# Kernel tuning notes

Measured on AMD Instinct MI355X. Metric: run time of the kernel, lower is better.

The kernel has to match this reference:

```python
import jax, jax.numpy as jnp
import numpy as np

B, T, C = 1, 4096, 2048
NH, HS, NQG = 16, 128, 4          # n_head, head_size, n_query_groups (GQA)
Q_PER_KV = NH // NQG              # 4
QKV_DIM = (NH + 2 * NQG) * HS     # 3072
ROT = HS // 2                     # rotary half-dim = 64


def setup_inputs() -> dict:
    key = jax.random.key(0)
    k0, k1, k2 = jax.random.split(key, 3)
    x = jax.random.normal(k0, (B, T, C), dtype=jnp.float32)
    W_attn = jax.random.normal(k1, (QKV_DIM, C), dtype=jnp.float32) * 0.02
    W_proj = jax.random.normal(k2, (C, C), dtype=jnp.float32) * 0.02
    # RoPE cache: cos/sin of shape (T, head_size/2), flash-attn convention
    inv_freq = 1.0 / (10000.0 ** (jnp.arange(0, HS, 2, dtype=jnp.float32) / HS))
    freqs = jnp.arange(T, dtype=jnp.float32)[:, None] * inv_freq[None, :]
    return {"x": x, "cos": jnp.cos(freqs), "sin": jnp.sin(freqs),
            "W_attn": W_attn, "W_proj": W_proj}


def _apply_rope(t, cos, sin):
    # t: (B, T, H, HS); cos/sin: (T, ROT). Non-interleaved (rotate-half) form.
    x1, x2 = t[..., :ROT], t[..., ROT:]
    c = cos[None, :, None, :]
    s = sin[None, :, None, :]
    return jnp.concatenate([x1 * c - x2 * s, x2 * c + x1 * s], axis=-1)


def reference(x, cos, sin, W_attn, W_proj):
    Bx, Tx, Cx = x.shape
    qkv = jnp.einsum('btc,fc->btf', x, W_attn)                 # (B,T,3072)
    qkv = qkv.reshape(Bx, Tx, NQG, Q_PER_KV + 2, HS)
    q = qkv[:, :, :, :Q_PER_KV, :].reshape(Bx, Tx, NH, HS)     # (B,T,16,128)
    k = qkv[:, :, :, Q_PER_KV, :]                              # (B,T,4,128)
    v = qkv[:, :, :, Q_PER_KV + 1, :]                          # (B,T,4,128)
    q = _apply_rope(q, cos, sin)
    k = _apply_rope(k, cos, sin)
    # GQA: expand kv groups to match query heads (repeat_interleave on head dim)
    k = jnp.repeat(k, Q_PER_KV, axis=2)                        # (B,T,16,128)
    v = jnp.repeat(v, Q_PER_KV, axis=2)
    scale = 1.0 / np.sqrt(HS).astype(np.float32)
    scores = jnp.einsum('bthd,bshd->bhts', q, k) * scale       # (B,H,T,T)
    causal = jnp.tril(jnp.ones((Tx, Tx), dtype=bool))
    scores = jnp.where(causal[None, None], scores, jnp.finfo(scores.dtype).min)
    attn = jax.nn.softmax(scores, axis=-1)
    y = jnp.einsum('bhts,bshd->bthd', attn, v).reshape(Bx, Tx, Cx)
    return jnp.einsum('btc,oc->bto', y, W_proj)
```

## Files before the change

kernel.cpp:

```cpp
#include <hip/hip_runtime.h>
#include <hip/hip_bf16.h>

typedef __hip_bfloat16 bf16;
typedef __attribute__((ext_vector_type(8))) short short8;
typedef __attribute__((ext_vector_type(4))) short short4v;
typedef __attribute__((ext_vector_type(4))) float floatx4;

#define T_SEQ 4096
#define C_DIM 2048
#define NHEAD 16
#define HSZ   128
#define NGRP  4

#define MFMA_BF16(A,B,C) __builtin_amdgcn_mfma_f32_16x16x32_bf16((A),(B),(C),0,0,0)

__device__ __forceinline__ void gld_lds16(const bf16* g, bf16* l) {
  __builtin_amdgcn_global_load_lds(
      (__attribute__((address_space(1))) void*)(g),
      (__attribute__((address_space(3))) void*)(l), 16, 0, 0);
}

__global__ void cvt_kernel(const float* __restrict__ src, bf16* __restrict__ dst, long n)
{
  const long i = ((long)blockIdx.x * blockDim.x + threadIdx.x) * 8;
  if (i >= n) return;
  const float4 a = *(const float4*)(src + i);
  const float4 b = *(const float4*)(src + i + 4);
  bf16 tmp[8];
  tmp[0] = __float2bfloat16(a.x); tmp[1] = __float2bfloat16(a.y);
  tmp[2] = __float2bfloat16(a.z); tmp[3] = __float2bfloat16(a.w);
  tmp[4] = __float2bfloat16(b.x); tmp[5] = __float2bfloat16(b.y);
  tmp[6] = __float2bfloat16(b.z); tmp[7] = __float2bfloat16(b.w);
  *(short8*)(dst + i) = *(const short8*)tmp;
}

__global__ __launch_bounds__(256, 3)
void gemm_bt_kernel(const bf16* __restrict__ A, const bf16* __restrict__ B,
                    float* __restrict__ Cf, bf16* __restrict__ Cq,
                    bf16* __restrict__ Ck, bf16* __restrict__ Cvt,
                    int K, int qkv_mode)
{
  __shared__ alignas(16) bf16 As[128 * 64];
  __shared__ alignas(16) bf16 Bs[128 * 64];

  const int t  = threadIdx.x;
  const int w  = t >> 6, l = t & 63;
  const int wr = w >> 1, wc = w & 1;
  const int q4 = l >> 4, ln = l & 15;
  const long bm = (long)blockIdx.y * 128;
  const long bn = (long)blockIdx.x * 128;

  floatx4 acc[4][4] = {};

  const bf16* Ab = A + (bm + t / 8) * (long)K + (t % 8) * 8;
  const bf16* Bb = B + (bn + t / 8) * (long)K + (t % 8) * 8;

  for (int k0 = 0; k0 < K; k0 += 64) {
    __syncthreads();
#pragma unroll
    for (int i = 0; i < 4; ++i) {
      gld_lds16(Ab + (long)i * 32 * K + k0, As + (i * 256 + w * 64) * 8);
      gld_lds16(Bb + (long)i * 32 * K + k0, Bs + (i * 256 + w * 64) * 8);
    }
    __syncthreads();
#pragma unroll
    for (int kk = 0; kk < 64; kk += 32) {
      short8 af[4], bfr[4];
      const int co = kk + q4 * 8;
#pragma unroll
      for (int mi = 0; mi < 4; ++mi)
        af[mi] = *(const short8*)(As + (wr * 64 + mi * 16 + ln) * 64 + co);
#pragma unroll
      for (int ni = 0; ni < 4; ++ni)
        bfr[ni] = *(const short8*)(Bs + (wc * 64 + ni * 16 + ln) * 64 + co);
#pragma unroll
      for (int mi = 0; mi < 4; ++mi)
#pragma unroll
        for (int ni = 0; ni < 4; ++ni)
          acc[mi][ni] = MFMA_BF16(af[mi], bfr[ni], acc[mi][ni]);
    }
  }

  if (!qkv_mode) {
#pragma unroll
    for (int mi = 0; mi < 4; ++mi) {
      const long r0 = bm + wr * 64 + mi * 16 + q4 * 4;
#pragma unroll
      for (int ni = 0; ni < 4; ++ni) {
        const long c = bn + wc * 64 + ni * 16 + ln;
#pragma unroll
        for (int r = 0; r < 4; ++r)
          Cf[(r0 + r) * C_DIM + c] = acc[mi][ni][r];
      }
    }
  } else {
    const int cb = blockIdx.x;
    const int g = cb / 6, slot = cb - g * 6;
    if (slot == 5) {
      bf16* dstv = Cvt + (long)g * HSZ * T_SEQ;
#pragma unroll
      for (int pass = 0; pass < 2; ++pass) {
        __syncthreads();
        if (wc == pass) {
#pragma unroll
          for (int mi = 0; mi < 4; ++mi) {
            const int tc = wr * 64 + mi * 16 + q4 * 4;
#pragma unroll
            for (int ni = 0; ni < 4; ++ni) {
              const int dr = ni * 16 + ln;
              short4v pk;
#pragma unroll
              for (int r = 0; r < 4; ++r) {
                bf16 v = __float2bfloat16(acc[mi][ni][r]);
                pk[r] = *(short*)&v;
              }
              *(short4v*)(As + dr * 128 + tc) = pk;
            }
          }
        }
        __syncthreads();
        const int row = t >> 2, ch = (t & 3) * 32;
        bf16* gp = dstv + (long)(pass * 64 + row) * T_SEQ + bm + ch;
#pragma unroll
        for (int jj = 0; jj < 4; ++jj)
          *(short8*)(gp + jj * 8) = *(const short8*)(As + row * 128 + ch + jj * 8);
      }
    } else {
      bf16* dst = (slot < 4) ? (Cq + (long)(g * 4 + slot) * T_SEQ * HSZ)
                             : (Ck + (long)g * T_SEQ * HSZ);
#pragma unroll
      for (int mi = 0; mi < 4; ++mi) {
        const long r0 = bm + wr * 64 + mi * 16 + q4 * 4;
#pragma unroll
        for (int ni = 0; ni < 4; ++ni) {
          const long c = wc * 64 + ni * 16 + ln;
#pragma unroll
          for (int r = 0; r < 4; ++r)
            dst[(r0 + r) * HSZ + c] = __float2bfloat16(acc[mi][ni][r]);
        }
      }
    }
  }
}

__global__ void rope_kernel(bf16* __restrict__ Q, bf16* __restrict__ Kb,
                            const float* __restrict__ cs, const float* __restrict__ sn)
{
  const long idx = (long)blockIdx.x * blockDim.x + threadIdx.x;
  const long NQ = (long)NHEAD * T_SEQ * 8;
  bf16* buf; long rem; float qs;
  if (idx < NQ) { buf = Q;  rem = idx;      qs = 0.08838834764831845f * 1.4426950408889634f; }
  else          { buf = Kb; rem = idx - NQ; qs = 1.0f; }
  const int d0 = (int)(rem & 7) * 8;
  const int tt = (int)((rem >> 3) & (T_SEQ - 1));
  const int hh = (int)(rem >> 15);
  const float4 c0 = *(const float4*)(cs + tt * 64 + d0);
  const float4 c1 = *(const float4*)(cs + tt * 64 + d0 + 4);
  const float4 s0 = *(const float4*)(sn + tt * 64 + d0);
  const float4 s1 = *(const float4*)(sn + tt * 64 + d0 + 4);
  float cc[8] = {c0.x,c0.y,c0.z,c0.w,c1.x,c1.y,c1.z,c1.w};
  float ss[8] = {s0.x,s0.y,s0.z,s0.w,s1.x,s1.y,s1.z,s1.w};
  bf16* p = buf + ((long)hh * T_SEQ + tt) * HSZ + d0;
  short8 v1 = *(const short8*)(p);
  short8 v2 = *(const short8*)(p + 64);
  short8 o1, o2;
#pragma unroll
  for (int jj = 0; jj < 8; ++jj) {
    short u1 = v1[jj], u2 = v2[jj];
    const float x1 = __bfloat162float(*(bf16*)&u1);
    const float x2 = __bfloat162float(*(bf16*)&u2);
    bf16 y1 = __float2bfloat16((x1 * cc[jj] - x2 * ss[jj]) * qs);
    bf16 y2 = __float2bfloat16((x2 * cc[jj] + x1 * ss[jj]) * qs);
    o1[jj] = *(short*)&y1; o2[jj] = *(short*)&y2;
  }
  *(short8*)(p)      = o1;
  *(short8*)(p + 64) = o2;
}

__global__ __launch_bounds__(256, 2)
void attn_kernel(const bf16* __restrict__ Qg, const bf16* __restrict__ Kg,
                 const bf16* __restrict__ Vtg, bf16* __restrict__ Y)
{
  __shared__ alignas(16) bf16 Ks[64][132];
  __shared__ alignas(16) bf16 Vt[128][68];
  __shared__ alignas(16) bf16 Ps[128][68];

  const int h = blockIdx.y;
  const int p = (blockIdx.y < 8) ? blockIdx.x : (31 - blockIdx.x);
  const int g = h >> 2;
  const int t = threadIdx.x;
  const int w = t >> 6, l = t & 63;
  const int q4 = l >> 4, ln = l & 15;

  const bf16* Qh = Qg + (long)h * T_SEQ * HSZ;
  const bf16* Kh = Kg + (long)g * T_SEQ * HSZ;
  const bf16* Vh = Vtg + (long)g * HSZ * T_SEQ;

  const int qbase = p * 128 + w * 32;

  short8 qf[2][4];
#pragma unroll
  for (int mi = 0; mi < 2; ++mi) {
    const long row = qbase + mi * 16 + ln;
#pragma unroll
    for (int ks = 0; ks < 4; ++ks)
      qf[mi][ks] = *(const short8*)(Qh + row * HSZ + ks * 32 + q4 * 8);
  }

  short8 ones_f;
#pragma unroll
  for (int i = 0; i < 8; ++i) ones_f[i] = (ln == 0) ? (short)0x3F80 : (short)0;

  floatx4 acc[2][8] = {};
  floatx4 acc_l[2] = {};

  const int krow = t >> 4, kc = (t & 15) * 8;
  const int vrow = t >> 3, vc = (t & 7) * 8;

  short8 kpre[4], vpre[4];
#pragma unroll
  for (int i = 0; i < 4; ++i) {
    kpre[i] = *(const short8*)(Kh + (long)(krow + 16 * i) * HSZ + kc);
    vpre[i] = *(const short8*)(Vh + (long)(vrow + 32 * i) * T_SEQ + vc);
  }

  const int jmax = 2 * p + 1;
  for (int j = 0; j <= jmax; ++j) {
    const int s0 = j * 64;
#pragma unroll
    for (int i = 0; i < 4; ++i) {
      *(short8*)(&Ks[krow + 16 * i][kc]) = kpre[i];
      *(short8*)(&Vt[vrow + 32 * i][vc]) = vpre[i];
    }
    __syncthreads();
    if (j < jmax) {
      const int s1 = s0 + 64;
#pragma unroll
      for (int i = 0; i < 4; ++i) {
        kpre[i] = *(const short8*)(Kh + (long)(s1 + krow + 16 * i) * HSZ + kc);
        vpre[i] = *(const short8*)(Vh + (long)(vrow + 32 * i) * T_SEQ + s1 + vc);
      }
    }

    if (s0 <= qbase + 31) {
      floatx4 sacc[2][4] = {};
#pragma unroll
      for (int ks = 0; ks < 4; ++ks) {
        short8 kf[4];
#pragma unroll
        for (int ni = 0; ni < 4; ++ni)
          kf[ni] = *(const short8*)(&Ks[ni * 16 + ln][ks * 32 + q4 * 8]);
#pragma unroll
        for (int mi = 0; mi < 2; ++mi)
#pragma unroll
          for (int ni = 0; ni < 4; ++ni)
            sacc[mi][ni] = MFMA_BF16(qf[mi][ks], kf[ni], sacc[mi][ni]);
      }

#pragma unroll
      for (int mi = 0; mi < 2; ++mi) {
        const int base_m = qbase + mi * 16 + q4 * 4 - s0 - ln;
#pragma unroll
        for (int ni = 0; ni < 4; ++ni)
#pragma unroll
          for (int r = 0; r < 4; ++r) {
            float pv = __builtin_amdgcn_exp2f(sacc[mi][ni][r]);
            if (base_m + r - ni * 16 < 0) pv = 0.f;
            Ps[w * 32 + mi * 16 + q4 * 4 + r][ni * 16 + ln] = __float2bfloat16(pv);
          }
      }

#pragma unroll
      for (int ks = 0; ks < 2; ++ks) {
        short8 pf[2], vf[8];
#pragma unroll
        for (int mi = 0; mi < 2; ++mi)
          pf[mi] = *(const short8*)(&Ps[w * 32 + mi * 16 + ln][ks * 32 + q4 * 8]);
#pragma unroll
        for (int nd = 0; nd < 8; ++nd)
          vf[nd] = *(const short8*)(&Vt[nd * 16 + ln][ks * 32 + q4 * 8]);
#pragma unroll
        for (int mi = 0; mi < 2; ++mi) {
          acc_l[mi] = MFMA_BF16(pf[mi], ones_f, acc_l[mi]);
#pragma unroll
          for (int nd = 0; nd < 8; ++nd)
            acc[mi][nd] = MFMA_BF16(pf[mi], vf[nd], acc[mi][nd]);
        }
      }
    }
    __syncthreads();
  }

#pragma unroll
  for (int mi = 0; mi < 2; ++mi) {
#pragma unroll
    for (int r = 0; r < 4; ++r) {
      const float lv = __shfl(acc_l[mi][r], l & 48, 64);
      const float inv = (lv > 0.f) ? 1.f / lv : 0.f;
      const long tq = qbase + mi * 16 + q4 * 4 + r;
#pragma unroll
      for (int nd = 0; nd < 8; ++nd)
        Y[tq * C_DIM + h * HSZ + nd * 16 + ln] = __float2bfloat16(acc[mi][nd][r] * inv);
    }
  }
}

extern "C" void kernel_launch(void* const* d_in, const int* in_sizes, int n_in,
                              void* d_out, int out_size, void* d_ws, size_t ws_size,
                              hipStream_t stream)
{
  const float* x  = (const float*)d_in[0];
  const float* cs = (const float*)d_in[1];
  const float* sn = (const float*)d_in[2];
  const float* Wa = (const float*)d_in[3];
  const float* Wp = (const float*)d_in[4];
  float* out = (float*)d_out;

  const long nx  = (long)T_SEQ * C_DIM;
  const long nwa = (long)(NHEAD + 2 * NGRP) * HSZ * C_DIM;
  const long nwp = (long)C_DIM * C_DIM;
  const long nqh = (long)NHEAD * T_SEQ * HSZ;
  const long nkg = (long)NGRP * T_SEQ * HSZ;

  const size_t need = (size_t)(nx + nwa + nqh + 2 * nkg + nqh) * sizeof(bf16);
  if (ws_size < need) return;

  bf16* xb  = (bf16*)d_ws;
  bf16* Wab = xb + nx;
  bf16* Q   = Wab + nwa;
  bf16* K   = Q + nqh;
  bf16* Vt  = K + nkg;
  bf16* Y   = Vt + nkg;
  bf16* Wpb = xb;

  cvt_kernel<<<(int)(nx  / 8 / 256), 256, 0, stream>>>(x,  xb,  nx);
  cvt_kernel<<<(int)(nwa / 8 / 256), 256, 0, stream>>>(Wa, Wab, nwa);
  gemm_bt_kernel<<<dim3(24, 32), 256, 0, stream>>>(xb, Wab, nullptr, Q, K, Vt, C_DIM, 1);
  rope_kernel<<<2560, 256, 0, stream>>>(Q, K, cs, sn);
  attn_kernel<<<dim3(32, NHEAD), 256, 0, stream>>>(Q, K, Vt, Y);
  cvt_kernel<<<(int)(nwp / 8 / 256), 256, 0, stream>>>(Wp, Wpb, nwp);
  gemm_bt_kernel<<<dim3(16, 32), 256, 0, stream>>>(Y, Wpb, out, nullptr, nullptr, nullptr, C_DIM, 0);
}
```

Measured before the change: 347.0 us.

## Shrink attention blocks to 64 queries with XCD-aware head mapping and shared K/P LDS

The attention kernel now uses 128-thread blocks covering 64 query rows, launched as 1024 blocks on a 1D grid. Block IDs are mapped so each XCD handles the heads of one KV group, which should improve L2 reuse of K/V, and causal tiles are paired front-to-back to balance load. The K tile and P tile now share one LDS buffer, separated by an extra barrier, which cuts LDS use so more blocks can be resident. In exchange, each K/V tile is reused by fewer queries and each tile pays an extra synchronisation.

Result: slower. 398.5 us (+14.8%).

```diff
diff --git a/kernel.cpp b/kernel.cpp
--- a/kernel.cpp
+++ b/kernel.cpp
@@ -177,17 +177,21 @@
   *(short8*)(p + 64) = o2;
 }
 
-__global__ __launch_bounds__(256, 2)
+__global__ __launch_bounds__(128, 2)
 void attn_kernel(const bf16* __restrict__ Qg, const bf16* __restrict__ Kg,
                  const bf16* __restrict__ Vtg, bf16* __restrict__ Y)
 {
-  __shared__ alignas(16) bf16 Ks[64][132];
+  __shared__ alignas(16) bf16 KsPs[64 * 132];
   __shared__ alignas(16) bf16 Vt[128][68];
-  __shared__ alignas(16) bf16 Ps[128][68];
-
-  const int h = blockIdx.y;
-  const int p = (blockIdx.y < 8) ? blockIdx.x : (31 - blockIdx.x);
-  const int g = h >> 2;
+
+  const int id  = blockIdx.x;
+  const int xcd = id & 7;
+  const int k   = id >> 3;
+  const int g   = xcd >> 1;
+  const int h   = g * 4 + (xcd & 1) * 2 + (k & 1);
+  const int si  = k >> 1;
+  const int S   = (si & 1) ? (63 - (si >> 1)) : (si >> 1);
+
   const int t = threadIdx.x;
   const int w = t >> 6, l = t & 63;
   const int q4 = l >> 4, ln = l & 15;
@@ -196,7 +200,7 @@
   const bf16* Kh = Kg + (long)g * T_SEQ * HSZ;
   const bf16* Vh = Vtg + (long)g * HSZ * T_SEQ;
 
-  const int qbase = p * 128 + w * 32;
+  const int qbase = S * 64 + w * 32;
 
   short8 qf[2][4];
 #pragma unroll
@@ -217,75 +221,74 @@
   const int krow = t >> 4, kc = (t & 15) * 8;
   const int vrow = t >> 3, vc = (t & 7) * 8;
 
-  short8 kpre[4], vpre[4];
-#pragma unroll
-  for (int i = 0; i < 4; ++i) {
-    kpre[i] = *(const short8*)(Kh + (long)(krow + 16 * i) * HSZ + kc);
-    vpre[i] = *(const short8*)(Vh + (long)(vrow + 32 * i) * T_SEQ + vc);
-  }
-
-  const int jmax = 2 * p + 1;
+  short8 kpre[8], vpre[8];
+#pragma unroll
+  for (int i = 0; i < 8; ++i) {
+    kpre[i] = *(const short8*)(Kh + (long)(krow + 8 * i) * HSZ + kc);
+    vpre[i] = *(const short8*)(Vh + (long)(vrow + 16 * i) * T_SEQ + vc);
+  }
+
+  const int jmax = S;
   for (int j = 0; j <= jmax; ++j) {
     const int s0 = j * 64;
 #pragma unroll
-    for (int i = 0; i < 4; ++i) {
-      *(short8*)(&Ks[krow + 16 * i][kc]) = kpre[i];
-      *(short8*)(&Vt[vrow + 32 * i][vc]) = vpre[i];
+    for (int i = 0; i < 8; ++i) {
+      *(short8*)(KsPs + (krow + 8 * i) * 132 + kc) = kpre[i];
+      *(short8*)(&Vt[vrow + 16 * i][vc]) = vpre[i];
     }
     __syncthreads();
     if (j < jmax) {
       const int s1 = s0 + 64;
 #pragma unroll
-      for (int i = 0; i < 4; ++i) {
-        kpre[i] = *(const short8*)(Kh + (long)(s1 + krow + 16 * i) * HSZ + kc);
-        vpre[i] = *(const short8*)(Vh + (long)(vrow + 32 * i) * T_SEQ + s1 + vc);
-      }
-    }
-
-    if (s0 <= qbase + 31) {
-      floatx4 sacc[2][4] = {};
-#pragma unroll
-      for (int ks = 0; ks < 4; ++ks) {
-        short8 kf[4];
+      for (int i = 0; i < 8; ++i) {
+        kpre[i] = *(const short8*)(Kh + (long)(s1 + krow + 8 * i) * HSZ + kc);
+        vpre[i] = *(const short8*)(Vh + (long)(vrow + 16 * i) * T_SEQ + s1 + vc);
+      }
+    }
+
+    floatx4 sacc[2][4] = {};
+#pragma unroll
+    for (int ks = 0; ks < 4; ++ks) {
+      short8 kf[4];
+#pragma unroll
+      for (int ni = 0; ni < 4; ++ni)
+        kf[ni] = *(const short8*)(KsPs + (ni * 16 + ln) * 132 + ks * 32 + q4 * 8);
+#pragma unroll
+      for (int mi = 0; mi < 2; ++mi)
 #pragma unroll
         for (int ni = 0; ni < 4; ++ni)
-          kf[ni] = *(const short8*)(&Ks[ni * 16 + ln][ks * 32 + q4 * 8]);
-#pragma unroll
-        for (int mi = 0; mi < 2; ++mi)
-#pragma unroll
-          for (int ni = 0; ni < 4; ++ni)
-            sacc[mi][ni] = MFMA_BF16(qf[mi][ks], kf[ni], sacc[mi][ni]);
-      }
-
+          sacc[mi][ni] = MFMA_BF16(qf[mi][ks], kf[ni], sacc[mi][ni]);
+    }
+    __syncthreads();
+
+#pragma unroll
+    for (int mi = 0; mi < 2; ++mi) {
+      const int base_m = qbase + mi * 16 + q4 * 4 - s0 - ln;
+#pragma unroll
+      for (int ni = 0; ni < 4; ++ni)
+#pragma unroll
+        for (int r = 0; r < 4; ++r) {
+          float pv = __builtin_amdgcn_exp2f(sacc[mi][ni][r]);
+          if (base_m + r - ni * 16 < 0) pv = 0.f;
+          KsPs[(w * 32 + mi * 16 + q4 * 4 + r) * 68 + ni * 16 + ln] = __float2bfloat16(pv);
+        }
+    }
+
+#pragma unroll
+    for (int ks = 0; ks < 2; ++ks) {
+      short8 pf[2], vf[8];
+#pragma unroll
+      for (int mi = 0; mi < 2; ++mi)
+        pf[mi] = *(const short8*)(KsPs + (w * 32 + mi * 16 + ln) * 68 + ks * 32 + q4 * 8);
+#pragma unroll
+      for (int nd = 0; nd < 8; ++nd)
+        vf[nd] = *(const short8*)(&Vt[nd * 16 + ln][ks * 32 + q4 * 8]);
 #pragma unroll
       for (int mi = 0; mi < 2; ++mi) {
-        const int base_m = qbase + mi * 16 + q4 * 4 - s0 - ln;
-#pragma unroll
-        for (int ni = 0; ni < 4; ++ni)
-#pragma unroll
-          for (int r = 0; r < 4; ++r) {
-            float pv = __builtin_amdgcn_exp2f(sacc[mi][ni][r]);
-            if (base_m + r - ni * 16 < 0) pv = 0.f;
-            Ps[w * 32 + mi * 16 + q4 * 4 + r][ni * 16 + ln] = __float2bfloat16(pv);
-          }
-      }
-
-#pragma unroll
-      for (int ks = 0; ks < 2; ++ks) {
-        short8 pf[2], vf[8];
-#pragma unroll
-        for (int mi = 0; mi < 2; ++mi)
-          pf[mi] = *(const short8*)(&Ps[w * 32 + mi * 16 + ln][ks * 32 + q4 * 8]);
+        acc_l[mi] = MFMA_BF16(pf[mi], ones_f, acc_l[mi]);
 #pragma unroll
         for (int nd = 0; nd < 8; ++nd)
-          vf[nd] = *(const short8*)(&Vt[nd * 16 + ln][ks * 32 + q4 * 8]);
-#pragma unroll
-        for (int mi = 0; mi < 2; ++mi) {
-          acc_l[mi] = MFMA_BF16(pf[mi], ones_f, acc_l[mi]);
-#pragma unroll
-          for (int nd = 0; nd < 8; ++nd)
-            acc[mi][nd] = MFMA_BF16(pf[mi], vf[nd], acc[mi][nd]);
-        }
+          acc[mi][nd] = MFMA_BF16(pf[mi], vf[nd], acc[mi][nd]);
       }
     }
     __syncthreads();
@@ -337,7 +340,7 @@
   cvt_kernel<<<(int)(nwa / 8 / 256), 256, 0, stream>>>(Wa, Wab, nwa);
   gemm_bt_kernel<<<dim3(24, 32), 256, 0, stream>>>(xb, Wab, nullptr, Q, K, Vt, C_DIM, 1);
   rope_kernel<<<2560, 256, 0, stream>>>(Q, K, cs, sn);
-  attn_kernel<<<dim3(32, NHEAD), 256, 0, stream>>>(Q, K, Vt, Y);
+  attn_kernel<<<1024, 128, 0, stream>>>(Q, K, Vt, Y);
   cvt_kernel<<<(int)(nwp / 8 / 256), 256, 0, stream>>>(Wp, Wpb, nwp);
   gemm_bt_kernel<<<dim3(16, 32), 256, 0, stream>>>(Y, Wpb, out, nullptr, nullptr, nullptr, C_DIM, 0);
 }
```

## Split long causal attention rows across blocks and merge partials in combine kernel

Applied to the files above, without the earlier changes.

Causal attention work is redistributed into 768 balanced blocks. Each head's 32 query tiles are grouped into pairs (c, 31-c), and the long tile's KV range is split across two blocks, so every block handles a similar number of KV steps. The split blocks write unnormalized bf16 partial outputs and row sums to workspace, and a new combine kernel adds them and normalizes. This aims to remove tail imbalance and improve CU occupancy, at the cost of an extra launch, partial-result traffic, and bf16 rounding of the partials.

New measurement: 372.1 us. +7.2%, slower.

```diff
diff --git a/kernel.cpp b/kernel.cpp
--- a/kernel.cpp
+++ b/kernel.cpp
@@ -179,15 +179,22 @@
 
 __global__ __launch_bounds__(256, 2)
 void attn_kernel(const bf16* __restrict__ Qg, const bf16* __restrict__ Kg,
-                 const bf16* __restrict__ Vtg, bf16* __restrict__ Y)
+                 const bf16* __restrict__ Vtg, bf16* __restrict__ Y,
+                 bf16* __restrict__ Opart, float* __restrict__ Lpart)
 {
   __shared__ alignas(16) bf16 Ks[64][132];
   __shared__ alignas(16) bf16 Vt[128][68];
   __shared__ alignas(16) bf16 Ps[128][68];
 
-  const int h = blockIdx.y;
-  const int p = (blockIdx.y < 8) ? blockIdx.x : (31 - blockIdx.x);
-  const int g = h >> 2;
+  const int id   = blockIdx.x;
+  const int h    = id / 48;
+  const int r48  = id - h * 48;
+  const int c    = r48 / 3, slot = r48 - c * 3;
+  const int P    = (slot == 0) ? c : (31 - c);
+  const int j0   = (slot == 2) ? (32 - c) : 0;
+  const int j1   = (slot == 0) ? (2 * c + 2) : ((slot == 1) ? (32 - c) : (64 - 2 * c));
+  const int g    = h >> 2;
+
   const int t = threadIdx.x;
   const int w = t >> 6, l = t & 63;
   const int q4 = l >> 4, ln = l & 15;
@@ -196,7 +203,7 @@
   const bf16* Kh = Kg + (long)g * T_SEQ * HSZ;
   const bf16* Vh = Vtg + (long)g * HSZ * T_SEQ;
 
-  const int qbase = p * 128 + w * 32;
+  const int qbase = P * 128 + w * 32;
 
   short8 qf[2][4];
 #pragma unroll
@@ -218,14 +225,16 @@
   const int vrow = t >> 3, vc = (t & 7) * 8;
 
   short8 kpre[4], vpre[4];
-#pragma unroll
-  for (int i = 0; i < 4; ++i) {
-    kpre[i] = *(const short8*)(Kh + (long)(krow + 16 * i) * HSZ + kc);
-    vpre[i] = *(const short8*)(Vh + (long)(vrow + 32 * i) * T_SEQ + vc);
-  }
-
-  const int jmax = 2 * p + 1;
-  for (int j = 0; j <= jmax; ++j) {
+  {
+    const int sb = j0 * 64;
+#pragma unroll
+    for (int i = 0; i < 4; ++i) {
+      kpre[i] = *(const short8*)(Kh + (long)(sb + krow + 16 * i) * HSZ + kc);
+      vpre[i] = *(const short8*)(Vh + (long)(vrow + 32 * i) * T_SEQ + sb + vc);
+    }
+  }
+
+  for (int j = j0; j < j1; ++j) {
     const int s0 = j * 64;
 #pragma unroll
     for (int i = 0; i < 4; ++i) {
@@ -233,7 +242,7 @@
       *(short8*)(&Vt[vrow + 32 * i][vc]) = vpre[i];
     }
     __syncthreads();
-    if (j < jmax) {
+    if (j + 1 < j1) {
       const int s1 = s0 + 64;
 #pragma unroll
       for (int i = 0; i < 4; ++i) {
@@ -242,66 +251,114 @@
       }
     }
 
-    if (s0 <= qbase + 31) {
-      floatx4 sacc[2][4] = {};
-#pragma unroll
-      for (int ks = 0; ks < 4; ++ks) {
-        short8 kf[4];
+    floatx4 sacc[2][4] = {};
+#pragma unroll
+    for (int ks = 0; ks < 4; ++ks) {
+      short8 kf[4];
+#pragma unroll
+      for (int ni = 0; ni < 4; ++ni)
+        kf[ni] = *(const short8*)(&Ks[ni * 16 + ln][ks * 32 + q4 * 8]);
+#pragma unroll
+      for (int mi = 0; mi < 2; ++mi)
 #pragma unroll
         for (int ni = 0; ni < 4; ++ni)
-          kf[ni] = *(const short8*)(&Ks[ni * 16 + ln][ks * 32 + q4 * 8]);
-#pragma unroll
-        for (int mi = 0; mi < 2; ++mi)
-#pragma unroll
-          for (int ni = 0; ni < 4; ++ni)
-            sacc[mi][ni] = MFMA_BF16(qf[mi][ks], kf[ni], sacc[mi][ni]);
-      }
-
+          sacc[mi][ni] = MFMA_BF16(qf[mi][ks], kf[ni], sacc[mi][ni]);
+    }
+
+#pragma unroll
+    for (int mi = 0; mi < 2; ++mi) {
+      const int base_m = qbase + mi * 16 + q4 * 4 - s0 - ln;
+#pragma unroll
+      for (int ni = 0; ni < 4; ++ni)
+#pragma unroll
+        for (int r = 0; r < 4; ++r) {
+          float pv = __builtin_amdgcn_exp2f(sacc[mi][ni][r]);
+          if (base_m + r - ni * 16 < 0) pv = 0.f;
+          Ps[w * 32 + mi * 16 + q4 * 4 + r][ni * 16 + ln] = __float2bfloat16(pv);
+        }
+    }
+
+#pragma unroll
+    for (int ks = 0; ks < 2; ++ks) {
+      short8 pf[2], vf[8];
+#pragma unroll
+      for (int mi = 0; mi < 2; ++mi)
+        pf[mi] = *(const short8*)(&Ps[w * 32 + mi * 16 + ln][ks * 32 + q4 * 8]);
+#pragma unroll
+      for (int nd = 0; nd < 8; ++nd)
+        vf[nd] = *(const short8*)(&Vt[nd * 16 + ln][ks * 32 + q4 * 8]);
 #pragma unroll
       for (int mi = 0; mi < 2; ++mi) {
-        const int base_m = qbase + mi * 16 + q4 * 4 - s0 - ln;
-#pragma unroll
-        for (int ni = 0; ni < 4; ++ni)
-#pragma unroll
-          for (int r = 0; r < 4; ++r) {
-            float pv = __builtin_amdgcn_exp2f(sacc[mi][ni][r]);
-            if (base_m + r - ni * 16 < 0) pv = 0.f;
-            Ps[w * 32 + mi * 16 + q4 * 4 + r][ni * 16 + ln] = __float2bfloat16(pv);
-          }
-      }
-
-#pragma unroll
-      for (int ks = 0; ks < 2; ++ks) {
-        short8 pf[2], vf[8];
-#pragma unroll
-        for (int mi = 0; mi < 2; ++mi)
-          pf[mi] = *(const short8*)(&Ps[w * 32 + mi * 16 + ln][ks * 32 + q4 * 8]);
+        acc_l[mi] = MFMA_BF16(pf[mi], ones_f, acc_l[mi]);
 #pragma unroll
         for (int nd = 0; nd < 8; ++nd)
-          vf[nd] = *(const short8*)(&Vt[nd * 16 + ln][ks * 32 + q4 * 8]);
-#pragma unroll
-        for (int mi = 0; mi < 2; ++mi) {
-          acc_l[mi] = MFMA_BF16(pf[mi], ones_f, acc_l[mi]);
-#pragma unroll
-          for (int nd = 0; nd < 8; ++nd)
-            acc[mi][nd] = MFMA_BF16(pf[mi], vf[nd], acc[mi][nd]);
-        }
+          acc[mi][nd] = MFMA_BF16(pf[mi], vf[nd], acc[mi][nd]);
       }
     }
     __syncthreads();
   }
 
-#pragma unroll
-  for (int mi = 0; mi < 2; ++mi) {
-#pragma unroll
-    for (int r = 0; r < 4; ++r) {
-      const float lv = __shfl(acc_l[mi][r], l & 48, 64);
-      const float inv = (lv > 0.f) ? 1.f / lv : 0.f;
-      const long tq = qbase + mi * 16 + q4 * 4 + r;
-#pragma unroll
-      for (int nd = 0; nd < 8; ++nd)
-        Y[tq * C_DIM + h * HSZ + nd * 16 + ln] = __float2bfloat16(acc[mi][nd][r] * inv);
-    }
+  if (slot == 0) {
+#pragma unroll
+    for (int mi = 0; mi < 2; ++mi) {
+#pragma unroll
+      for (int r = 0; r < 4; ++r) {
+        const float lv = __shfl(acc_l[mi][r], l & 48, 64);
+        const float inv = (lv > 0.f) ? 1.f / lv : 0.f;
+        const long tq = qbase + mi * 16 + q4 * 4 + r;
+#pragma unroll
+        for (int nd = 0; nd < 8; ++nd)
+          Y[tq * C_DIM + h * HSZ + nd * 16 + ln] = __float2bfloat16(acc[mi][nd][r] * inv);
+      }
+    }
+  } else {
+    const int sidx = (h * 16 + (P - 16)) * 2 + (slot - 1);
+    bf16* Op = Opart + (long)sidx * (128 * 128);
+    float* Lp = Lpart + sidx * 128;
+#pragma unroll
+    for (int mi = 0; mi < 2; ++mi) {
+#pragma unroll
+      for (int r = 0; r < 4; ++r) {
+        const int row = w * 32 + mi * 16 + q4 * 4 + r;
+        if (ln == 0) Lp[row] = acc_l[mi][r];
+#pragma unroll
+        for (int nd = 0; nd < 8; ++nd)
+          Op[row * 128 + nd * 16 + ln] = __float2bfloat16(acc[mi][nd][r]);
+      }
+    }
+  }
+}
+
+__global__ void combine_kernel(const bf16* __restrict__ Opart,
+                               const float* __restrict__ Lpart,
+                               bf16* __restrict__ Y)
+{
+  const int b = blockIdx.x;
+  const int h = b >> 4, pp = b & 15;
+  const bf16* O0 = Opart + (long)b * 2 * 16384;
+  const bf16* O1 = O0 + 16384;
+  const float* L0 = Lpart + b * 256;
+  const float* L1 = L0 + 128;
+  const long qb = (long)(pp + 16) * 128;
+  const int t = threadIdx.x;
+#pragma unroll
+  for (int it = 0; it < 8; ++it) {
+    const int idx = it * 2048 + t * 8;
+    const int row = idx >> 7, d = idx & 127;
+    const float lsum = L0[row] + L1[row];
+    const float inv = (lsum > 0.f) ? 1.f / lsum : 0.f;
+    const short8 a = *(const short8*)(O0 + idx);
+    const short8 bb = *(const short8*)(O1 + idx);
+    short8 o;
+#pragma unroll
+    for (int jj = 0; jj < 8; ++jj) {
+      short ua = a[jj], ub = bb[jj];
+      const float fa = __bfloat162float(*(bf16*)&ua);
+      const float fb = __bfloat162float(*(bf16*)&ub);
+      bf16 y = __float2bfloat16((fa + fb) * inv);
+      o[jj] = *(short*)&y;
+    }
+    *(short8*)(Y + (qb + row) * C_DIM + h * HSZ + d) = o;
   }
 }
 
@@ -331,13 +388,16 @@
   bf16* K   = Q + nqh;
   bf16* Vt  = K + nkg;
   bf16* Y   = Vt + nkg;
-  bf16* Wpb = xb;
+  bf16* Wpb = Q;
+  bf16* Opart = xb;
+  float* Lpart = (float*)Wab;
 
   cvt_kernel<<<(int)(nx  / 8 / 256), 256, 0, stream>>>(x,  xb,  nx);
   cvt_kernel<<<(int)(nwa / 8 / 256), 256, 0, stream>>>(Wa, Wab, nwa);
   gemm_bt_kernel<<<dim3(24, 32), 256, 0, stream>>>(xb, Wab, nullptr, Q, K, Vt, C_DIM, 1);
   rope_kernel<<<2560, 256, 0, stream>>>(Q, K, cs, sn);
-  attn_kernel<<<dim3(32, NHEAD), 256, 0, stream>>>(Q, K, Vt, Y);
+  attn_kernel<<<768, 256, 0, stream>>>(Q, K, Vt, Y, Opart, Lpart);
+  combine_kernel<<<256, 256, 0, stream>>>(Opart, Lpart, Y);
   cvt_kernel<<<(int)(nwp / 8 / 256), 256, 0, stream>>>(Wp, Wpb, nwp);
   gemm_bt_kernel<<<dim3(16, 32), 256, 0, stream>>>(Y, Wpb, out, nullptr, nullptr, nullptr, C_DIM, 0);
 }
```
